# Optimization experiments

Measured on AMD Instinct MI355X. Metric: run time of the kernel, lower is better.

## Reference

```python
import math
import jax, jax.numpy as jnp
import numpy as np

S, B, K, D, T, MAX_LEN = 2048, 128, 64, 256, 6, 2048
LOG_2PI = math.log(2.0 * math.pi)


def _make_pe(d_model, max_len):
    position = np.arange(max_len, dtype=np.float32)[:, None]
    div_term = np.exp(np.arange(0, d_model, 2, dtype=np.float32) * (-math.log(10000.0) / d_model))
    pe = np.zeros((max_len, 1, d_model), dtype=np.float32)
    pe[:, 0, 0::2] = np.sin(position * div_term)
    pe[:, 0, 1::2] = np.cos(position * div_term)  # d_model even
    return jnp.asarray(pe)


def setup_inputs() -> dict:
    key = jax.random.key(0)
    k1, k2, k3, k4, k5 = jax.random.split(key, 5)
    traj_feats = jax.random.normal(k1, (S, B, T), dtype=jnp.float32)
    xy_coords = jax.random.normal(k2, (S, B, 2), dtype=jnp.float32)
    means = jax.random.normal(k3, (K, 2), dtype=jnp.float32)          # key centers
    A = jax.random.normal(k4, (K, 2, 2), dtype=jnp.float32)          # PSD factor: cov = A A^T
    W = jax.random.normal(k5, (D, K), dtype=jnp.float32) * (1.0 / math.sqrt(K))  # Linear weight
    b = jnp.zeros((D,), dtype=jnp.float32)
    pe = _make_pe(D, MAX_LEN)
    return {"traj_feats": traj_feats, "xy_coords": xy_coords,
            "means": means, "A": A, "W": W, "b": b, "pe": pe}


def reference(traj_feats, xy_coords, means, A, W, b, pe):
    # Batched 2x2 Gaussian log-prob over all keys (fused, closed-form).
    cov = jnp.einsum('kij,klj->kil', A, A)                    # (K,2,2) = A A^T
    det = cov[:, 0, 0] * cov[:, 1, 1] - cov[:, 0, 1] * cov[:, 1, 0]  # (K,)
    inv = jnp.stack([
        jnp.stack([cov[:, 1, 1], -cov[:, 0, 1]], axis=-1),
        jnp.stack([-cov[:, 1, 0], cov[:, 0, 0]], axis=-1),
    ], axis=-2) / det[:, None, None]                          # (K,2,2)
    diff = xy_coords[:, :, None, :] - means                   # (S,B,K,2)
    quad = jnp.einsum('sbki,kij,sbkj->sbk', diff, inv, diff)  # Mahalanobis^2
    log_weights = -0.5 * (quad + jnp.log(det) + 2.0 * LOG_2PI)  # (S,B,K)
    # Weighted-sum embedding (Linear over key axis) + positional encoding.
    emb = jnp.einsum('sbk,dk->sbd', log_weights, W) + b       # (S,B,D)
    emb = emb + pe[:emb.shape[0]]                             # pe: (max_len,1,D)
    # dropout layers are identity at inference
    return jnp.concatenate([traj_feats, emb], axis=-1)        # (S,B,T+D)
```

## Files before the change

kernel.cpp:

```cpp
#include <hip/hip_runtime.h>
#include <math.h>

#define S_DIM 2048
#define B_DIM 128
#define K_DIM 64
#define D_DIM 256
#define T_DIM 6
#define ROW_LEN (T_DIM + D_DIM)
#define LOG_2PI_F 1.8378770664093453f
#define RPB 16

__global__ __launch_bounds__(256) void coef_kernel(
    const float* __restrict__ means,
    const float* __restrict__ A,
    const float* __restrict__ W,
    const float* __restrict__ bvec,
    float* __restrict__ Mt)
{
    __shared__ float c[6][K_DIM];
    int t = threadIdx.x;
    if (t < K_DIM) {
        float a00 = A[4*t+0], a01 = A[4*t+1], a10 = A[4*t+2], a11 = A[4*t+3];
        float cov00 = a00*a00 + a01*a01;
        float cov01 = a00*a10 + a01*a11;
        float cov11 = a10*a10 + a11*a11;
        float det   = cov00*cov11 - cov01*cov01;
        float rdet  = 1.0f / det;
        float i00 =  cov11*rdet, i01 = -cov01*rdet, i11 = cov00*rdet;
        float mx = means[2*t], my = means[2*t+1];
        c[0][t] = -0.5f*(i00*mx*mx + 2.0f*i01*mx*my + i11*my*my + logf(det)) - LOG_2PI_F;
        c[1][t] = i00*mx + i01*my;
        c[2][t] = i01*mx + i11*my;
        c[3][t] = -0.5f*i00;
        c[4][t] = -i01;
        c[5][t] = -0.5f*i11;
    }
    __syncthreads();
    int d = t;
    float m0 = 0.f, m1 = 0.f, m2 = 0.f, m3 = 0.f, m4 = 0.f, m5 = 0.f;
    const float* wrow = W + d*K_DIM;
#pragma unroll
    for (int k = 0; k < K_DIM; ++k) {
        float w = wrow[k];
        m0 += w*c[0][k]; m1 += w*c[1][k]; m2 += w*c[2][k];
        m3 += w*c[3][k]; m4 += w*c[4][k]; m5 += w*c[5][k];
    }
    Mt[0*D_DIM + d] = m0 + bvec[d];
    Mt[1*D_DIM + d] = m1;
    Mt[2*D_DIM + d] = m2;
    Mt[3*D_DIM + d] = m3;
    Mt[4*D_DIM + d] = m4;
    Mt[5*D_DIM + d] = m5;
}

__global__ __launch_bounds__(256) void emb_kernel(
    const float* __restrict__ traj,
    const float* __restrict__ xy,
    const float* __restrict__ pe,
    const float* __restrict__ Mt,
    float* __restrict__ out)
{
    int t    = threadIdx.x;
    int row0 = blockIdx.x * RPB;
    int s    = row0 >> 7;
    float m0 = Mt[0*D_DIM + t], m1 = Mt[1*D_DIM + t], m2 = Mt[2*D_DIM + t];
    float m3 = Mt[3*D_DIM + t], m4 = Mt[4*D_DIM + t], m5 = Mt[5*D_DIM + t];
    float p  = pe[s*D_DIM + t];
#pragma unroll
    for (int r = 0; r < RPB; ++r) {
        int row = row0 + r;
        float x = xy[2*row + 0];
        float y = xy[2*row + 1];
        float v = m0 + m1*x + m2*y + (m3*x + m4*y)*x + m5*y*y + p;
        size_t base = (size_t)row * ROW_LEN;
        out[base + T_DIM + t] = v;
        if (t < T_DIM) out[base + t] = traj[row*T_DIM + t];
    }
}

extern "C" void kernel_launch(void* const* d_in, const int* in_sizes, int n_in,
                              void* d_out, int out_size, void* d_ws, size_t ws_size,
                              hipStream_t stream) {
    const float* traj  = (const float*)d_in[0];
    const float* xy    = (const float*)d_in[1];
    const float* means = (const float*)d_in[2];
    const float* A     = (const float*)d_in[3];
    const float* W     = (const float*)d_in[4];
    const float* bvec  = (const float*)d_in[5];
    const float* pe    = (const float*)d_in[6];
    float* out = (float*)d_out;
    float* Mt  = (float*)d_ws;

    coef_kernel<<<1, 256, 0, stream>>>(means, A, W, bvec, Mt);

    int nrows = S_DIM * B_DIM;
    int grid  = nrows / RPB;
    emb_kernel<<<grid, 256, 0, stream>>>(traj, xy, pe, Mt, out);
}
```

Measured before the change: 352.6 us.

## Stage output rows in shared memory and store them with coalesced float4 writes

The embedding kernel now writes a block's 16 output rows, including the interleaved trajectory features, into a shared-memory tile. It then copies the contiguous tile to global memory with aligned float4 stores, which replaces the misaligned per-row scalar stores. The xy and trajectory inputs are loaded once per block with vector loads. The positional encoding is folded into the constant term. The cost is the extra shared memory, two block barriers and one more pass through LDS.

```diff
diff --git a/kernel.cpp b/kernel.cpp
--- a/kernel.cpp
+++ b/kernel.cpp
@@ -60,22 +60,50 @@
     const float* __restrict__ Mt,
     float* __restrict__ out)
 {
+    __shared__ float tile[RPB * ROW_LEN];
+    __shared__ float xys[2 * RPB];
+
     int t    = threadIdx.x;
-    int row0 = blockIdx.x * RPB;
+    int blk  = blockIdx.x;
+    int row0 = blk * RPB;
     int s    = row0 >> 7;
-    float m0 = Mt[0*D_DIM + t], m1 = Mt[1*D_DIM + t], m2 = Mt[2*D_DIM + t];
+
+    if (t < 8) {
+        float4 v = ((const float4*)xy)[blk * 8 + t];
+        ((float4*)xys)[t] = v;
+    }
+    if (t >= 64 && t < 88) {
+        int i = t - 64;
+        float4 v = ((const float4*)traj)[blk * 24 + i];
+        int j = i * 4;
+        tile[(j    / T_DIM) * ROW_LEN + (j    % T_DIM)] = v.x;
+        tile[((j+1)/ T_DIM) * ROW_LEN + ((j+1)% T_DIM)] = v.y;
+        tile[((j+2)/ T_DIM) * ROW_LEN + ((j+2)% T_DIM)] = v.z;
+        tile[((j+3)/ T_DIM) * ROW_LEN + ((j+3)% T_DIM)] = v.w;
+    }
+
+    float m0 = Mt[0*D_DIM + t] + pe[s*D_DIM + t];
+    float m1 = Mt[1*D_DIM + t], m2 = Mt[2*D_DIM + t];
     float m3 = Mt[3*D_DIM + t], m4 = Mt[4*D_DIM + t], m5 = Mt[5*D_DIM + t];
-    float p  = pe[s*D_DIM + t];
+
+    __syncthreads();
+
 #pragma unroll
     for (int r = 0; r < RPB; ++r) {
-        int row = row0 + r;
-        float x = xy[2*row + 0];
-        float y = xy[2*row + 1];
-        float v = m0 + m1*x + m2*y + (m3*x + m4*y)*x + m5*y*y + p;
-        size_t base = (size_t)row * ROW_LEN;
-        out[base + T_DIM + t] = v;
-        if (t < T_DIM) out[base + t] = traj[row*T_DIM + t];
+        float x = xys[2*r], y = xys[2*r + 1];
+        float v = m0 + m1*x + m2*y + (m3*x + m4*y)*x + m5*y*y;
+        tile[r * ROW_LEN + T_DIM + t] = v;
     }
+
+    __syncthreads();
+
+    const float4* t4 = (const float4*)tile;
+    float4* o4 = (float4*)(out + (size_t)row0 * ROW_LEN);
+#pragma unroll
+    for (int k = 0; k < 4; ++k)
+        o4[k * 256 + t] = t4[k * 256 + t];
+    if (t < 24)
+        o4[1024 + t] = t4[1024 + t];
 }
 
 extern "C" void kernel_launch(void* const* d_in, const int* in_sizes, int n_in,
```

After: 296.6 us. 15.9% less time.
